# Performance work log

Hardware: AMD Instinct MI355X
Metric: run time of the kernel (lower is better)

## Reference

```python
import jax, jax.numpy as jnp
import numpy as np

# Model constants (match init_kwargs)
B, V, NUM_NODES, NUM_RELS = 32, 20, 4000, 400
EMB, HID, L, N, E, OUT = 128, 128, 3, 32000, 256000, 128
DECAY = 0.03
EPS = 0.0  # self_attn eps, not trained


def setup_inputs() -> dict:
    key = jax.random.key(0)
    ks = jax.random.split(key, 20)
    s = 0.02
    return {
        "node_ids": jax.random.randint(ks[0], (N,), 0, NUM_NODES),
        "rel_ids": jax.random.randint(ks[1], (E,), 0, NUM_RELS),
        "edge_index": jax.random.randint(ks[2], (2, E), 0, N),
        "batch": jnp.sort(jax.random.randint(ks[3], (N,), 0, B)),
        "visit_node": jax.random.uniform(ks[4], (B, V, NUM_NODES), dtype=jnp.float32),
        "ehr_nodes": jax.random.uniform(ks[5], (B, NUM_NODES), dtype=jnp.float32),
        "node_emb": jax.random.normal(ks[6], (NUM_NODES, EMB), dtype=jnp.float32) * s,
        "rel_emb": jax.random.normal(ks[7], (NUM_RELS, EMB), dtype=jnp.float32) * s,
        "lin_w": jax.random.normal(ks[8], (HID, EMB), dtype=jnp.float32) * s,
        "lin_b": jnp.zeros((HID,), jnp.float32),
        "alpha_w": jax.random.normal(ks[9], (L, NUM_NODES, NUM_NODES), dtype=jnp.float32) * 0.002,
        "alpha_b": jnp.zeros((L, NUM_NODES), jnp.float32),
        "beta_w": jax.random.normal(ks[10], (L, 1, NUM_NODES), dtype=jnp.float32) * s,
        "beta_b": jnp.zeros((L, 1), jnp.float32),
        "wr_w": jax.random.normal(ks[11], (L, 1, HID), dtype=jnp.float32) * s,
        "wr_b": jnp.zeros((L, 1), jnp.float32),
        "nn_w": jax.random.normal(ks[12], (L, HID, HID), dtype=jnp.float32) * s,
        "nn_b": jnp.zeros((L, HID), jnp.float32),
        "mlp_w": jax.random.normal(ks[13], (OUT, 2 * HID), dtype=jnp.float32) * s,
        "mlp_b": jnp.zeros((OUT,), jnp.float32),
    }


def reference(node_ids, rel_ids, edge_index, batch, visit_node, ehr_nodes,
              node_emb, rel_emb, lin_w, lin_b, alpha_w, alpha_b, beta_w, beta_b,
              wr_w, wr_b, nn_w, nn_b, mlp_w, mlp_b):
    # visit decay weights lambda_j: (1, V, 1)
    lambda_j = jnp.exp(DECAY * (V - jnp.arange(V, dtype=jnp.float32))).reshape(1, V, 1)

    x = node_emb[node_ids] @ lin_w.T + lin_b          # (N, HID)
    edge_attr = rel_emb[rel_ids] @ lin_w.T + lin_b    # (E, HID)
    src, dst = edge_index[0], edge_index[1]
    nid_src = node_ids[src]
    b_src = batch[src]

    for l in range(L):
        # alpha: softmax over visit dim, (B, V, NUM_NODES)
        alpha = jax.nn.softmax(
            jnp.einsum('bvn,mn->bvm', visit_node, alpha_w[l]) + alpha_b[l], axis=1)
        # beta: (B, V, 1) with visit decay
        beta = jnp.tanh(
            jnp.einsum('bvn,on->bvo', visit_node, beta_w[l]) + beta_b[l]) * lambda_j
        attn = jnp.sum(alpha * beta, axis=1)          # (B, NUM_NODES)
        e_attn = attn[b_src, nid_src][:, None]        # (E, 1) per-edge attention

        # BiAttentionGNNConv message: relu(x_j * attn + W_R(edge_attr) * edge_attr)
        w_rel = edge_attr @ wr_w[l].T + wr_b[l]       # (E, 1)
        msg = jax.nn.relu(x[src] * e_attn + w_rel * edge_attr)
        agg = jax.ops.segment_sum(msg, dst, num_segments=N)  # scatter-add aggregate
        out = agg + (1.0 + EPS) * x                   # eps residual
        x = jax.nn.relu(out @ nn_w[l].T + nn_b[l])    # conv.nn Linear + outer relu

    # graph-level patient embedding: global mean pool over batch
    counts = jnp.maximum(
        jax.ops.segment_sum(jnp.ones((N, 1), x.dtype), batch, num_segments=B), 1.0)
    x_graph = jax.ops.segment_sum(x, batch, num_segments=B) / counts  # (B, HID)

    # node-level patient embedding: ehr multihot average of node embeddings
    x_node = (ehr_nodes @ node_emb) / jnp.sum(ehr_nodes, axis=1, keepdims=True)
    x_node = x_node @ lin_w.T + lin_b                 # (B, HID)

    logits = jnp.concatenate([x_graph, x_node], axis=1) @ mlp_w.T + mlp_b
    return logits
```

## Files before the change

kernel.cpp:

```cpp
#include <hip/hip_runtime.h>

namespace {

constexpr int kNodes = 4000;
constexpr int kRels  = 400;
constexpr int kB     = 32;
constexpr int kV     = 20;
constexpr int kN     = 32000;
constexpr int kE     = 256000;
constexpr int kH     = 128;
constexpr int kL     = 3;
constexpr int kMPad  = 4096;
constexpr int kBV    = kB * kV;
constexpr int kNB    = 32;
constexpr int kChunk = kE / kNB;
constexpr int kHalf  = 16000;

typedef __attribute__((ext_vector_type(8))) short bf16x8;
typedef __attribute__((ext_vector_type(4))) float f32x4;

__device__ inline unsigned short f2bf(float f){
  unsigned int u = __float_as_uint(f);
  u += 0x7FFFu + ((u >> 16) & 1u);
  return (unsigned short)(u >> 16);
}

__device__ inline void gload_lds16(const unsigned short* g, unsigned short* l){
  __builtin_amdgcn_global_load_lds(
      (const __attribute__((address_space(1))) unsigned int*)(g),
      (__attribute__((address_space(3))) unsigned int*)(l),
      16, 0, 0);
}


__global__ void transpose_kernel(const float* __restrict__ lin_w, const float* __restrict__ nn_w,
                                 float* __restrict__ lin_wT, float* __restrict__ nn_wT){
  int m = blockIdx.x;
  const float* in = (m == 0) ? lin_w : nn_w + (size_t)(m-1)*kH*kH;
  float* out      = (m == 0) ? lin_wT : nn_wT + (size_t)(m-1)*kH*kH;
  for (int i = threadIdx.x; i < kH*kH; i += blockDim.x){
    int r = i >> 7, c = i & (kH-1);
    out[c*kH + r] = in[i];
  }
}

__global__ __launch_bounds__(128) void proj_kernel(const float* __restrict__ node_emb,
    const float* __restrict__ rel_emb, const float* __restrict__ lin_wT,
    const float* __restrict__ lin_b, float* __restrict__ emb_lin, float* __restrict__ rel_lin){
  int row = blockIdx.x;
  const float* src; float* dst;
  if (row < kNodes){ src = node_emb + (size_t)row*kH; dst = emb_lin + (size_t)row*kH; }
  else             { src = rel_emb + (size_t)(row-kNodes)*kH; dst = rel_lin + (size_t)(row-kNodes)*kH; }
  __shared__ float rs[kH];
  int h = threadIdx.x;
  rs[h] = src[h];
  __syncthreads();
  float acc = lin_b[h];
#pragma unroll 8
  for (int k = 0; k < kH; k++) acc = fmaf(rs[k], lin_wT[k*kH + h], acc);
  dst[h] = acc;
}

__global__ void gather_x0_kernel(const int* __restrict__ node_ids,
                                 const float* __restrict__ emb_lin, float* __restrict__ x){
  int idx = blockIdx.x*256 + threadIdx.x;
  if (idx < kN*kH){
    int i = idx >> 7, c = idx & (kH-1);
    x[idx] = emb_lin[(size_t)node_ids[i]*kH + c];
  }
}

__global__ __launch_bounds__(128) void relterm_kernel(const float* __restrict__ rel_lin,
    const float* __restrict__ wr_w, const float* __restrict__ wr_b, float* __restrict__ relterm){
  int l = blockIdx.x / kRels, r = blockIdx.x % kRels;
  int t = threadIdx.x;
  float rl = rel_lin[(size_t)r*kH + t];
  __shared__ float red[kH];
  red[t] = rl * wr_w[l*kH + t];
  __syncthreads();
  for (int o = 64; o > 0; o >>= 1){
    if (t < o) red[t] += red[t+o];
    __syncthreads();
  }
  float w = red[0] + wr_b[l];
  relterm[((size_t)l*kRels + r)*kH + t] = w * rl;
}


__global__ __launch_bounds__(256) void csr_hist_kernel(const int* __restrict__ dst,
    unsigned short* __restrict__ rank, unsigned int* __restrict__ hpart){
  __shared__ unsigned int hb[kHalf];
  int p = blockIdx.x;
  int base = blockIdx.y * kHalf;
  int t = threadIdx.x;
  for (int i = t; i < kHalf; i += 256) hb[i] = 0u;
  __syncthreads();
  for (int i = t; i < kChunk; i += 256){
    int e = p*kChunk + i;
    int d = dst[e];
    int rel = d - base;
    if ((unsigned)rel < (unsigned)kHalf){
      rank[e] = (unsigned short)atomicAdd(&hb[rel], 1u);
    }
  }
  __syncthreads();
  for (int i = t; i < kHalf; i += 256)
    hpart[(size_t)p*kN + base + i] = hb[i];
}

__global__ __launch_bounds__(256) void csr_col_kernel(unsigned int* __restrict__ hpart,
    int* __restrict__ deg){
  int bin = blockIdx.x*256 + threadIdx.x;
  if (bin >= kN) return;
  unsigned int s = 0;
#pragma unroll
  for (int p = 0; p < kNB; p++){
    size_t idx = (size_t)p*kN + bin;
    unsigned int v = hpart[idx];
    hpart[idx] = s;
    s += v;
  }
  deg[bin] = (int)s;
}

__global__ __launch_bounds__(256) void scanA_kernel(const int* __restrict__ deg,
    int* __restrict__ starts, int* __restrict__ bsum){
  __shared__ int buf[256];
  int gid = blockIdx.x*256 + threadIdx.x;
  int t = threadIdx.x;
  int v = (gid < kN) ? deg[gid] : 0;
  buf[t] = v;
  __syncthreads();
  for (int o = 1; o < 256; o <<= 1){
    int add = (t >= o) ? buf[t-o] : 0;
    __syncthreads();
    buf[t] += add;
    __syncthreads();
  }
  if (gid < kN) starts[gid] = buf[t] - v;
  if (t == 255) bsum[blockIdx.x] = buf[255];
}

__global__ __launch_bounds__(128) void scanB_kernel(const int* __restrict__ bsum,
    int* __restrict__ boffs, int nblk){
  __shared__ int buf[128];
  int t = threadIdx.x;
  int v = (t < nblk) ? bsum[t] : 0;
  buf[t] = v;
  __syncthreads();
  for (int o = 1; o < 128; o <<= 1){
    int add = (t >= o) ? buf[t-o] : 0;
    __syncthreads();
    buf[t] += add;
    __syncthreads();
  }
  if (t < nblk) boffs[t] = buf[t] - v;
}

__global__ __launch_bounds__(256) void scanC_kernel(int* __restrict__ starts,
    const int* __restrict__ boffs){
  int gid = blockIdx.x*256 + threadIdx.x;
  if (gid < kN) starts[gid] += boffs[blockIdx.x];
  if (gid == kN-1) starts[kN] = kE;
}

__global__ __launch_bounds__(256) void csr_place_kernel(const int* __restrict__ dst,
    const int* __restrict__ starts, const unsigned int* __restrict__ colOff,
    const unsigned short* __restrict__ rank, int* __restrict__ perm){
  int blk = blockIdx.x;
  int p = blk >> 2;
  for (int i = threadIdx.x; i < 2000; i += 256){
    int e = blk*2000 + i;
    int d = dst[e];
    int pos = starts[d] + (int)colOff[(size_t)p*kN + d] + (int)rank[e];
    perm[pos] = e;
  }
}

__global__ void ub_kernel(const int* __restrict__ batch, int* __restrict__ ub){
  int j = threadIdx.x;
  if (j > kB) return;
  int lo = 0, hi = kN;
  while (lo < hi){
    int mid = (lo + hi) >> 1;
    if (batch[mid] < j) lo = mid + 1; else hi = mid;
  }
  ub[j] = lo;
}


__global__ void cvt_visit_kernel(const float* __restrict__ visit, unsigned short* __restrict__ out){
  int i = blockIdx.x*256 + threadIdx.x;
  if (i >= kBV*kNodes/8) return;
  const float4 a = *reinterpret_cast<const float4*>(visit + (size_t)i*8);
  const float4 b = *reinterpret_cast<const float4*>(visit + (size_t)i*8 + 4);
  unsigned short r[8] = {f2bf(a.x),f2bf(a.y),f2bf(a.z),f2bf(a.w),
                         f2bf(b.x),f2bf(b.y),f2bf(b.z),f2bf(b.w)};
  *reinterpret_cast<uint4*>(out + (size_t)i*8) = *reinterpret_cast<uint4*>(r);
}

__global__ void cvtW_kernel(const float* __restrict__ W, unsigned short* __restrict__ out){
  int i = blockIdx.x*256 + threadIdx.x;
  constexpr int perL = kMPad*(kNodes/8);
  if (i >= kL*perL) return;
  int l = i / perL;
  int rem = i - l*perL;
  int row = rem / (kNodes/8);
  int col = (rem - row*(kNodes/8)) * 8;
  unsigned short r[8];
  if (row < kNodes){
    const float* p = W + (size_t)l*kNodes*kNodes + (size_t)row*kNodes + col;
    const float4 a = *reinterpret_cast<const float4*>(p);
    const float4 b = *reinterpret_cast<const float4*>(p + 4);
    r[0]=f2bf(a.x); r[1]=f2bf(a.y); r[2]=f2bf(a.z); r[3]=f2bf(a.w);
    r[4]=f2bf(b.x); r[5]=f2bf(b.y); r[6]=f2bf(b.z); r[7]=f2bf(b.w);
  } else {
    for (int q = 0; q < 8; q++) r[q] = 0;
  }
  *reinterpret_cast<uint4*>(out + (size_t)l*kMPad*kNodes + (size_t)row*kNodes + col)
      = *reinterpret_cast<uint4*>(r);
}

__global__ __launch_bounds__(256) void gemm_bt_bf16(const unsigned short* __restrict__ A,
    const unsigned short* __restrict__ Ball, float* __restrict__ Sbase){
  __shared__ unsigned short As[128*32];
  __shared__ unsigned short Bs[128*32];
  int bm = blockIdx.x, bn = blockIdx.y;
  int lz = blockIdx.z;
  int l = lz >> 1, z = lz & 1;
  const unsigned short* B = Ball + (size_t)l*kMPad*kNodes;
  float* C = Sbase + (size_t)lz*kBV*kMPad;
  int kBeg = z ? 2016 : 0;
  int kEnd = z ? kNodes : 2016;
  int t = threadIdx.x;
  int lane = t & 63, wave = t >> 6;
  int wm = (wave >> 1) * 64, wn = (wave & 1) * 64;
  int r = lane & 15, g = lane >> 4;

  int srow = wave*32 + (lane >> 2);
  int sk   = (lane & 3) * 8;
  const unsigned short* Ag = A + (size_t)(bm*128 + srow)*kNodes + kBeg + sk;
  const unsigned short* Bg = B + (size_t)(bn*128 + srow)*kNodes + kBeg + sk;
  unsigned short* AsB0 = &As[(wave*32    )*32];
  unsigned short* AsB1 = &As[(wave*32 + 16)*32];
  unsigned short* BsB0 = &Bs[(wave*32    )*32];
  unsigned short* BsB1 = &Bs[(wave*32 + 16)*32];
  const size_t rowStep = (size_t)16*kNodes;

  f32x4 acc[4][4];
#pragma unroll
  for (int i = 0; i < 4; i++)
#pragma unroll
    for (int j = 0; j < 4; j++) acc[i][j] = f32x4{0.f,0.f,0.f,0.f};

  for (int k0 = kBeg; k0 < kEnd; k0 += 32){
    __syncthreads();
    gload_lds16(Ag,           AsB0);
    gload_lds16(Ag + rowStep, AsB1);
    gload_lds16(Bg,           BsB0);
    gload_lds16(Bg + rowStep, BsB1);
    Ag += 32; Bg += 32;
    __syncthreads();
    bf16x8 af[4], bf[4];
#pragma unroll
    for (int i = 0; i < 4; i++){
      af[i] = *reinterpret_cast<const bf16x8*>(&As[(wm + i*16 + r)*32 + g*8]);
      bf[i] = *reinterpret_cast<const bf16x8*>(&Bs[(wn + i*16 + r)*32 + g*8]);
    }
#pragma unroll
    for (int i = 0; i < 4; i++)
#pragma unroll
      for (int j = 0; j < 4; j++)
        acc[i][j] = __builtin_amdgcn_mfma_f32_16x16x32_bf16(af[i], bf[j], acc[i][j], 0, 0, 0);
  }
#pragma unroll
  for (int i = 0; i < 4; i++)
#pragma unroll
    for (int j = 0; j < 4; j++){
      int row = bm*128 + wm + i*16 + g*4;
      int col = bn*128 + wn + j*16 + r;
#pragma unroll
      for (int q = 0; q < 4; q++)
        C[(size_t)(row + q)*kMPad + col] = acc[i][j][q];
    }
}

__global__ __launch_bounds__(256) void beta_all_kernel(const float* __restrict__ visit,
    const float* __restrict__ beta_w, const float* __restrict__ beta_b,
    float* __restrict__ beta){
  int wid = (blockIdx.x*256 + threadIdx.x) >> 6;
  int lane = threadIdx.x & 63;
  if (wid >= kL*kBV) return;
  int l = wid / kBV, bv = wid - l*kBV;
  const float* row = visit + (size_t)bv*kNodes;
  const float* bw = beta_w + (size_t)l*kNodes;
  float s = 0.f;
  for (int k = lane; k < kNodes; k += 64) s = fmaf(row[k], bw[k], s);
#pragma unroll
  for (int o = 32; o > 0; o >>= 1) s += __shfl_down(s, o);
  if (lane == 0){
    int v = bv % kV;
    float lam = __expf(0.03f * (float)(kV - v));
    beta[wid] = tanhf(s + beta_b[l]) * lam;
  }
}

__global__ __launch_bounds__(256) void attn_kernel(const float* __restrict__ S,
    const float* __restrict__ beta, float* __restrict__ attn){
  int idx = blockIdx.x*256 + threadIdx.x;
  if (idx >= kL*kB*kNodes) return;
  int l = idx / (kB*kNodes);
  int rem = idx - l*(kB*kNodes);
  int b = rem / kNodes;
  int m = rem - b*kNodes;
  const float* S0 = S + (size_t)(l*2)*kBV*kMPad + (size_t)b*kV*kMPad + m;
  const float* S1 = S0 + (size_t)kBV*kMPad;
  float vals[kV];
  float mx = -1e30f;
#pragma unroll
  for (int v = 0; v < kV; v++){
    float s = S0[(size_t)v*kMPad] + S1[(size_t)v*kMPad];
    vals[v] = s; mx = fmaxf(mx, s);
  }
  float se = 0.f, ws = 0.f;
  const float* bp = beta + l*kBV + b*kV;
#pragma unroll
  for (int v = 0; v < kV; v++){ float e = __expf(vals[v] - mx); se += e; ws = fmaf(e, bp[v], ws); }
  attn[idx] = ws / se;
}

__global__ void attn_gather_kernel(const int* __restrict__ batch,
    const int* __restrict__ node_ids, const float* __restrict__ attn,
    float* __restrict__ att_n){
  int idx = blockIdx.x*256 + threadIdx.x;
  if (idx >= kL*kN) return;
  int l = idx / kN, n = idx - l*kN;
  att_n[idx] = attn[(size_t)l*kB*kNodes + (size_t)batch[n]*kNodes + node_ids[n]];
}


__global__ __launch_bounds__(256) void agg_kernel(const int* __restrict__ starts,
    const int* __restrict__ perm, const int* __restrict__ src, const int* __restrict__ rel_ids,
    const float* __restrict__ att_n_l, const float* __restrict__ relterm_l,
    const float* __restrict__ x, float* __restrict__ agg){
  int wid = (blockIdx.x*256 + threadIdx.x) >> 6;
  int lane = threadIdx.x & 63;
  if (wid >= kN) return;
  int p0 = starts[wid], p1 = starts[wid+1];
  int c = lane*2;
  float a0 = 0.f, a1 = 0.f;
  for (int p = p0; p < p1; p++){
    int e = perm[p];
    int s = src[e];
    float at = att_n_l[s];
    float2 xv = *reinterpret_cast<const float2*>(&x[(size_t)s*kH + c]);
    float2 rt = *reinterpret_cast<const float2*>(&relterm_l[(size_t)rel_ids[e]*kH + c]);
    float m0 = fmaf(xv.x, at, rt.x); m0 = m0 > 0.f ? m0 : 0.f;
    float m1 = fmaf(xv.y, at, rt.y); m1 = m1 > 0.f ? m1 : 0.f;
    a0 += m0; a1 += m1;
  }
  *reinterpret_cast<float2*>(&agg[(size_t)wid*kH + c]) = float2{a0, a1};
}

__global__ __launch_bounds__(256) void nn_kernel(const float* __restrict__ agg,
    float* __restrict__ x, const float* __restrict__ nn_wT_l, const float* __restrict__ nn_b_l){
  __shared__ float rows[8][kH];
  int rb = blockIdx.x * 8;
  int t = threadIdx.x;
#pragma unroll
  for (int i = 0; i < 4; i++){
    int idx = t + i*256;
    int rr = idx >> 7, cc = idx & (kH-1);
    size_t gi = (size_t)(rb + rr)*kH + cc;
    rows[rr][cc] = agg[gi] + x[gi];
  }
  __syncthreads();
  int cc = t & (kH-1);
  int r0 = (t >> 7) * 4;
  float acc0 = 0.f, acc1 = 0.f, acc2 = 0.f, acc3 = 0.f;
#pragma unroll 8
  for (int k = 0; k < kH; k++){
    float w = nn_wT_l[k*kH + cc];
    acc0 = fmaf(rows[r0+0][k], w, acc0);
    acc1 = fmaf(rows[r0+1][k], w, acc1);
    acc2 = fmaf(rows[r0+2][k], w, acc2);
    acc3 = fmaf(rows[r0+3][k], w, acc3);
  }
  float b = nn_b_l[cc];
  x[(size_t)(rb+r0+0)*kH + cc] = fmaxf(acc0 + b, 0.f);
  x[(size_t)(rb+r0+1)*kH + cc] = fmaxf(acc1 + b, 0.f);
  x[(size_t)(rb+r0+2)*kH + cc] = fmaxf(acc2 + b, 0.f);
  x[(size_t)(rb+r0+3)*kH + cc] = fmaxf(acc3 + b, 0.f);
}


__global__ __launch_bounds__(128) void pool_part_kernel(const float* __restrict__ x,
    const int* __restrict__ ub, float* __restrict__ pp){
  int s = blockIdx.x, b = blockIdx.y, c = threadIdx.x;
  int lo = ub[b], len = ub[b+1] - lo;
  int i0 = lo + (int)(((long long)len * s) >> 3);
  int i1 = lo + (int)(((long long)len * (s+1)) >> 3);
  float acc = 0.f;
  for (int i = i0; i < i1; i++) acc += x[(size_t)i*kH + c];
  pp[(size_t)(b*8 + s)*kH + c] = acc;
}

__global__ __launch_bounds__(128) void xnode1_kernel(const float* __restrict__ ehr,
    const float* __restrict__ node_emb, float* __restrict__ pn, float* __restrict__ ps){
  int s = blockIdx.x, b = blockIdx.y, c = threadIdx.x;
  int n0 = s * (kNodes/8), n1 = n0 + (kNodes/8);
  float acc = 0.f, es = 0.f;
  for (int n = n0; n < n1; n++){
    float e = ehr[(size_t)b*kNodes + n];
    es += e;
    acc = fmaf(e, node_emb[(size_t)n*kH + c], acc);
  }
  pn[(size_t)(b*8 + s)*kH + c] = acc;
  if (c == 0) ps[b*8 + s] = es;
}

__global__ __launch_bounds__(128) void readout_kernel(const float* __restrict__ pp,
    const int* __restrict__ ub, const float* __restrict__ pn, const float* __restrict__ ps,
    const float* __restrict__ lin_wT, const float* __restrict__ lin_b,
    const float* __restrict__ mlp_w, const float* __restrict__ mlp_b,
    float* __restrict__ out){
  int b = blockIdx.x, h = threadIdx.x;
  __shared__ float v[2*kH];
  __shared__ float ts[kH];
  float s = 0.f;
#pragma unroll
  for (int q = 0; q < 8; q++) s += pp[(size_t)(b*8 + q)*kH + h];
  int len = ub[b+1] - ub[b]; if (len < 1) len = 1;
  v[h] = s / (float)len;
  float acc = 0.f, es = 0.f;
#pragma unroll
  for (int q = 0; q < 8; q++){
    acc += pn[(size_t)(b*8 + q)*kH + h];
    es  += ps[b*8 + q];
  }
  ts[h] = acc / es;
  __syncthreads();
  float r = lin_b[h];
#pragma unroll 8
  for (int k = 0; k < kH; k++) r = fmaf(ts[k], lin_wT[k*kH + h], r);
  v[kH + h] = r;
  __syncthreads();
  float o = mlp_b[h];
#pragma unroll 8
  for (int k = 0; k < 2*kH; k++) o = fmaf(v[k], mlp_w[(size_t)h*2*kH + k], o);
  out[b*kH + h] = o;
}

}

extern "C" void kernel_launch(void* const* d_in, const int* in_sizes, int n_in,
                              void* d_out, int out_size, void* d_ws, size_t ws_size,
                              hipStream_t stream){
  const int*   node_ids = (const int*)d_in[0];
  const int*   rel_ids  = (const int*)d_in[1];
  const int*   e_src    = (const int*)d_in[2];
  const int*   e_dst    = e_src + kE;
  const int*   batch    = (const int*)d_in[3];
  const float* visit    = (const float*)d_in[4];
  const float* ehr      = (const float*)d_in[5];
  const float* node_emb = (const float*)d_in[6];
  const float* rel_emb  = (const float*)d_in[7];
  const float* lin_w    = (const float*)d_in[8];
  const float* lin_b    = (const float*)d_in[9];
  const float* alpha_w  = (const float*)d_in[10];
  const float* beta_w   = (const float*)d_in[12];
  const float* beta_b   = (const float*)d_in[13];
  const float* wr_w     = (const float*)d_in[14];
  const float* wr_b     = (const float*)d_in[15];
  const float* nn_w     = (const float*)d_in[16];
  const float* nn_b     = (const float*)d_in[17];
  const float* mlp_w    = (const float*)d_in[18];
  const float* mlp_b    = (const float*)d_in[19];
  float* out = (float*)d_out;

  char* w = (char*)d_ws;
  auto alloc = [&](size_t bytes)->char*{
    char* p = w; w += (bytes + 255) & ~(size_t)255; return p;
  };
  int*   starts = (int*)  alloc((size_t)(kN+1)*4);
  int*   deg    = (int*)  alloc((size_t)kN*4);
  int*   bsum   = (int*)  alloc(256*4);
  int*   boffs  = (int*)  alloc(256*4);
  int*   ub     = (int*)  alloc((kB+1)*4);
  int*   perm   = (int*)  alloc((size_t)kE*4);
  unsigned short* rank = (unsigned short*)alloc((size_t)kE*2);
  unsigned int* hpart  = (unsigned int*)alloc((size_t)kNB*kN*4);
  float* embLin = (float*)alloc((size_t)kNodes*kH*4);
  float* relLin = (float*)alloc((size_t)kRels*kH*4);
  float* relterm= (float*)alloc((size_t)kL*kRels*kH*4);
  float* linwT  = (float*)alloc((size_t)kH*kH*4);
  float* nnwT   = (float*)alloc((size_t)kL*kH*kH*4);
  float* x      = (float*)alloc((size_t)kN*kH*4);
  float* agg    = (float*)alloc((size_t)kN*kH*4);
  unsigned short* visitbf = (unsigned short*)alloc((size_t)kBV*kNodes*2);
  unsigned short* awbf    = (unsigned short*)alloc((size_t)kL*kMPad*kNodes*2);
  float* S      = (float*)alloc((size_t)kL*2*kBV*kMPad*4);
  float* attn   = (float*)alloc((size_t)kL*kB*kNodes*4);
  float* att_n  = (float*)alloc((size_t)kL*kN*4);
  float* beta   = (float*)alloc((size_t)kL*kBV*4);
  float* pp     = (float*)alloc((size_t)kB*8*kH*4);
  float* pn     = (float*)alloc((size_t)kB*8*kH*4);
  float* ps     = (float*)alloc((size_t)kB*8*4);
  if ((size_t)(w - (char*)d_ws) > ws_size) return;

  transpose_kernel<<<4, 256, 0, stream>>>(lin_w, nn_w, linwT, nnwT);
  proj_kernel<<<kNodes + kRels, 128, 0, stream>>>(node_emb, rel_emb, linwT, lin_b, embLin, relLin);
  gather_x0_kernel<<<(kN*kH)/256, 256, 0, stream>>>(node_ids, embLin, x);
  relterm_kernel<<<kL*kRels, 128, 0, stream>>>(relLin, wr_w, wr_b, relterm);

  csr_hist_kernel<<<dim3(kNB, 2), 256, 0, stream>>>(e_dst, rank, hpart);
  csr_col_kernel<<<(kN+255)/256, 256, 0, stream>>>(hpart, deg);
  scanA_kernel<<<(kN+255)/256, 256, 0, stream>>>(deg, starts, bsum);
  scanB_kernel<<<1, 128, 0, stream>>>(bsum, boffs, (kN+255)/256);
  scanC_kernel<<<(kN+255)/256, 256, 0, stream>>>(starts, boffs);
  csr_place_kernel<<<128, 256, 0, stream>>>(e_dst, starts, hpart, rank, perm);
  ub_kernel<<<1, 64, 0, stream>>>(batch, ub);

  cvt_visit_kernel<<<(kBV*kNodes/8 + 255)/256, 256, 0, stream>>>(visit, visitbf);
  beta_all_kernel<<<kL*kBV/4, 256, 0, stream>>>(visit, beta_w, beta_b, beta);
  cvtW_kernel<<<(kL*kMPad*(kNodes/8) + 255)/256, 256, 0, stream>>>(alpha_w, awbf);
  gemm_bt_bf16<<<dim3(kBV/128, kMPad/128, kL*2), 256, 0, stream>>>(visitbf, awbf, S);
  attn_kernel<<<(kL*kB*kNodes + 255)/256, 256, 0, stream>>>(S, beta, attn);
  attn_gather_kernel<<<(kL*kN + 255)/256, 256, 0, stream>>>(batch, node_ids, attn, att_n);

  for (int l = 0; l < kL; l++){
    agg_kernel<<<kN/4, 256, 0, stream>>>(starts, perm, e_src, rel_ids,
        att_n + (size_t)l*kN, relterm + (size_t)l*kRels*kH, x, agg);
    nn_kernel<<<kN/8, 256, 0, stream>>>(agg, x, nnwT + (size_t)l*kH*kH, nn_b + (size_t)l*kH);
  }

  pool_part_kernel<<<dim3(8, kB), 128, 0, stream>>>(x, ub, pp);
  xnode1_kernel<<<dim3(8, kB), 128, 0, stream>>>(ehr, node_emb, pn, ps);
  readout_kernel<<<kB, 128, 0, stream>>>(pp, ub, pn, ps, linwT, lin_b, mlp_w, mlp_b, out);
}
```

Before: 632.9 us.

## Pad GEMM K to 4096, use 64-wide K tiles with XOR-swizzled LDS and block remap

Pads the bf16 visit and alpha_w copies along K to 4096 so each split-K half covers exactly 2048. The GEMM now stages 64-wide K tiles per barrier pair instead of 32, halving the number of synchronizations. It also XOR-swizzles the LDS layout to avoid bank conflicts, and remaps the 1D grid so blocks are spread across XCDs. The cost is extra zero-padding work and memory in the conversion kernels, plus more LDS per block.

```diff
diff --git a/kernel.cpp b/kernel.cpp
--- a/kernel.cpp
+++ b/kernel.cpp
@@ -11,6 +11,7 @@
 constexpr int kH     = 128;
 constexpr int kL     = 3;
 constexpr int kMPad  = 4096;
+constexpr int kKPad  = 4096;
 constexpr int kBV    = kB * kV;
 constexpr int kNB    = 32;
 constexpr int kChunk = kE / kNB;
@@ -191,24 +192,32 @@
 
 __global__ void cvt_visit_kernel(const float* __restrict__ visit, unsigned short* __restrict__ out){
   int i = blockIdx.x*256 + threadIdx.x;
-  if (i >= kBV*kNodes/8) return;
-  const float4 a = *reinterpret_cast<const float4*>(visit + (size_t)i*8);
-  const float4 b = *reinterpret_cast<const float4*>(visit + (size_t)i*8 + 4);
-  unsigned short r[8] = {f2bf(a.x),f2bf(a.y),f2bf(a.z),f2bf(a.w),
-                         f2bf(b.x),f2bf(b.y),f2bf(b.z),f2bf(b.w)};
-  *reinterpret_cast<uint4*>(out + (size_t)i*8) = *reinterpret_cast<uint4*>(r);
+  if (i >= kBV*(kKPad/8)) return;
+  int row = i >> 9;
+  int col = (i & 511) * 8;
+  unsigned short r[8];
+  if (col < kNodes){
+    const float* p = visit + (size_t)row*kNodes + col;
+    const float4 a = *reinterpret_cast<const float4*>(p);
+    const float4 b = *reinterpret_cast<const float4*>(p + 4);
+    r[0]=f2bf(a.x); r[1]=f2bf(a.y); r[2]=f2bf(a.z); r[3]=f2bf(a.w);
+    r[4]=f2bf(b.x); r[5]=f2bf(b.y); r[6]=f2bf(b.z); r[7]=f2bf(b.w);
+  } else {
+    for (int q = 0; q < 8; q++) r[q] = 0;
+  }
+  *reinterpret_cast<uint4*>(out + (size_t)row*kKPad + col) = *reinterpret_cast<uint4*>(r);
 }
 
 __global__ void cvtW_kernel(const float* __restrict__ W, unsigned short* __restrict__ out){
   int i = blockIdx.x*256 + threadIdx.x;
-  constexpr int perL = kMPad*(kNodes/8);
+  constexpr int perL = kMPad*(kKPad/8);
   if (i >= kL*perL) return;
   int l = i / perL;
   int rem = i - l*perL;
-  int row = rem / (kNodes/8);
-  int col = (rem - row*(kNodes/8)) * 8;
+  int row = rem >> 9;
+  int col = (rem & 511) * 8;
   unsigned short r[8];
-  if (row < kNodes){
+  if (row < kNodes && col < kNodes){
     const float* p = W + (size_t)l*kNodes*kNodes + (size_t)row*kNodes + col;
     const float4 a = *reinterpret_cast<const float4*>(p);
     const float4 b = *reinterpret_cast<const float4*>(p + 4);
@@ -217,35 +226,34 @@
   } else {
     for (int q = 0; q < 8; q++) r[q] = 0;
   }
-  *reinterpret_cast<uint4*>(out + (size_t)l*kMPad*kNodes + (size_t)row*kNodes + col)
+  *reinterpret_cast<uint4*>(out + (size_t)l*kMPad*kKPad + (size_t)row*kKPad + col)
       = *reinterpret_cast<uint4*>(r);
 }
 
 __global__ __launch_bounds__(256) void gemm_bt_bf16(const unsigned short* __restrict__ A,
     const unsigned short* __restrict__ Ball, float* __restrict__ Sbase){
-  __shared__ unsigned short As[128*32];
-  __shared__ unsigned short Bs[128*32];
-  int bm = blockIdx.x, bn = blockIdx.y;
-  int lz = blockIdx.z;
+  __shared__ unsigned short As[128*64];
+  __shared__ unsigned short Bs[128*64];
+  int wg = (blockIdx.x & 7)*120 + (blockIdx.x >> 3);
+  int lz = wg / 160;
+  int rem = wg - lz*160;
+  int bn = rem / 5;
+  int bm = rem - bn*5;
   int l = lz >> 1, z = lz & 1;
-  const unsigned short* B = Ball + (size_t)l*kMPad*kNodes;
+  const unsigned short* B = Ball + (size_t)l*kMPad*kKPad;
   float* C = Sbase + (size_t)lz*kBV*kMPad;
-  int kBeg = z ? 2016 : 0;
-  int kEnd = z ? kNodes : 2016;
+  int kBase = z * 2048;
+
   int t = threadIdx.x;
   int lane = t & 63, wave = t >> 6;
   int wm = (wave >> 1) * 64, wn = (wave & 1) * 64;
   int r = lane & 15, g = lane >> 4;
 
-  int srow = wave*32 + (lane >> 2);
-  int sk   = (lane & 3) * 8;
-  const unsigned short* Ag = A + (size_t)(bm*128 + srow)*kNodes + kBeg + sk;
-  const unsigned short* Bg = B + (size_t)(bn*128 + srow)*kNodes + kBeg + sk;
-  unsigned short* AsB0 = &As[(wave*32    )*32];
-  unsigned short* AsB1 = &As[(wave*32 + 16)*32];
-  unsigned short* BsB0 = &Bs[(wave*32    )*32];
-  unsigned short* BsB1 = &Bs[(wave*32 + 16)*32];
-  const size_t rowStep = (size_t)16*kNodes;
+  int ri = lane >> 3, s = lane & 7;
+  int koff = ((s ^ ri) << 3);
+  const unsigned short* Ag = A + (size_t)(bm*128 + wave*32 + ri)*kKPad + kBase + koff;
+  const unsigned short* Bg = B + (size_t)(bn*128 + wave*32 + ri)*kKPad + kBase + koff;
+  const size_t chunkStep = (size_t)8*kKPad;
 
   f32x4 acc[4][4];
 #pragma unroll
@@ -253,25 +261,32 @@
 #pragma unroll
     for (int j = 0; j < 4; j++) acc[i][j] = f32x4{0.f,0.f,0.f,0.f};
 
-  for (int k0 = kBeg; k0 < kEnd; k0 += 32){
-    __syncthreads();
-    gload_lds16(Ag,           AsB0);
-    gload_lds16(Ag + rowStep, AsB1);
-    gload_lds16(Bg,           BsB0);
-    gload_lds16(Bg + rowStep, BsB1);
-    Ag += 32; Bg += 32;
-    __syncthreads();
-    bf16x8 af[4], bf[4];
-#pragma unroll
-    for (int i = 0; i < 4; i++){
-      af[i] = *reinterpret_cast<const bf16x8*>(&As[(wm + i*16 + r)*32 + g*8]);
-      bf[i] = *reinterpret_cast<const bf16x8*>(&Bs[(wn + i*16 + r)*32 + g*8]);
+  for (int k0 = 0; k0 < 2048; k0 += 64){
+    __syncthreads();
+#pragma unroll
+    for (int c = 0; c < 4; c++){
+      gload_lds16(Ag + c*chunkStep, &As[(wave*32 + c*8)*64]);
+      gload_lds16(Bg + c*chunkStep, &Bs[(wave*32 + c*8)*64]);
     }
-#pragma unroll
-    for (int i = 0; i < 4; i++)
-#pragma unroll
-      for (int j = 0; j < 4; j++)
-        acc[i][j] = __builtin_amdgcn_mfma_f32_16x16x32_bf16(af[i], bf[j], acc[i][j], 0, 0, 0);
+    Ag += 64; Bg += 64;
+    __syncthreads();
+#pragma unroll
+    for (int ksub = 0; ksub < 2; ksub++){
+      bf16x8 af[4], bf[4];
+#pragma unroll
+      for (int i = 0; i < 4; i++){
+        int arow = wm + i*16 + r;
+        int brow = wn + i*16 + r;
+        int slot = ((ksub << 2) + g);
+        af[i] = *reinterpret_cast<const bf16x8*>(&As[arow*64 + ((slot ^ (arow & 7)) << 3)]);
+        bf[i] = *reinterpret_cast<const bf16x8*>(&Bs[brow*64 + ((slot ^ (brow & 7)) << 3)]);
+      }
+#pragma unroll
+      for (int i = 0; i < 4; i++)
+#pragma unroll
+        for (int j = 0; j < 4; j++)
+          acc[i][j] = __builtin_amdgcn_mfma_f32_16x16x32_bf16(af[i], bf[j], acc[i][j], 0, 0, 0);
+    }
   }
 #pragma unroll
   for (int i = 0; i < 4; i++)
@@ -497,8 +512,8 @@
   float* nnwT   = (float*)alloc((size_t)kL*kH*kH*4);
   float* x      = (float*)alloc((size_t)kN*kH*4);
   float* agg    = (float*)alloc((size_t)kN*kH*4);
-  unsigned short* visitbf = (unsigned short*)alloc((size_t)kBV*kNodes*2);
-  unsigned short* awbf    = (unsigned short*)alloc((size_t)kL*kMPad*kNodes*2);
+  unsigned short* visitbf = (unsigned short*)alloc((size_t)kBV*kKPad*2);
+  unsigned short* awbf    = (unsigned short*)alloc((size_t)kL*kMPad*kKPad*2);
   float* S      = (float*)alloc((size_t)kL*2*kBV*kMPad*4);
   float* attn   = (float*)alloc((size_t)kL*kB*kNodes*4);
   float* att_n  = (float*)alloc((size_t)kL*kN*4);
@@ -521,10 +536,10 @@
   csr_place_kernel<<<128, 256, 0, stream>>>(e_dst, starts, hpart, rank, perm);
   ub_kernel<<<1, 64, 0, stream>>>(batch, ub);
 
-  cvt_visit_kernel<<<(kBV*kNodes/8 + 255)/256, 256, 0, stream>>>(visit, visitbf);
+  cvt_visit_kernel<<<(kBV*(kKPad/8) + 255)/256, 256, 0, stream>>>(visit, visitbf);
   beta_all_kernel<<<kL*kBV/4, 256, 0, stream>>>(visit, beta_w, beta_b, beta);
-  cvtW_kernel<<<(kL*kMPad*(kNodes/8) + 255)/256, 256, 0, stream>>>(alpha_w, awbf);
-  gemm_bt_bf16<<<dim3(kBV/128, kMPad/128, kL*2), 256, 0, stream>>>(visitbf, awbf, S);
+  cvtW_kernel<<<(kL*kMPad*(kKPad/8) + 255)/256, 256, 0, stream>>>(alpha_w, awbf);
+  gemm_bt_bf16<<<960, 256, 0, stream>>>(visitbf, awbf, S);
   attn_kernel<<<(kL*kB*kNodes + 255)/256, 256, 0, stream>>>(S, beta, attn);
   attn_gather_kernel<<<(kL*kN + 255)/256, 256, 0, stream>>>(batch, node_ids, attn, att_n);
 
```

Measured after the change: 610.7 us. 3.5% less time.
